# Optimization experiments

Hardware: AMD Instinct MI355X
Metric: run time of the kernel (lower is better)

The kernel has to match this reference:

```python
import jax, jax.numpy as jnp
import numpy as np

B, T, D_IN, D_OUT, H = 128, 128, 64, 64, 1024


def _lstm_cell(x_t, h, c, W_ih, W_hh, b_ih, b_hh):
    # PyTorch LSTMCell: gates = x@W_ih^T + b_ih + h@W_hh^T + b_hh, order [i, f, g, o]
    g = x_t @ W_ih.T + b_ih + h @ W_hh.T + b_hh  # [B, 4H]
    i, f, gg, o = jnp.split(g, 4, axis=-1)
    c_new = jax.nn.sigmoid(f) * c + jax.nn.sigmoid(i) * jnp.tanh(gg)
    h_new = jax.nn.sigmoid(o) * jnp.tanh(c_new)
    return h_new, c_new


def setup_inputs() -> dict:
    key = jax.random.key(0)
    ks = jax.random.split(key, 16)
    s_in = 1.0 / np.sqrt(H)
    inp = {
        "x": jax.random.normal(ks[0], (B, T, D_IN), dtype=jnp.float32),
        "W_ih1": jax.random.normal(ks[1], (4 * H, D_IN), dtype=jnp.float32) * s_in,
        "W_hh1": jax.random.normal(ks[2], (4 * H, H), dtype=jnp.float32) * s_in,
        "b_ih1": jax.random.normal(ks[3], (4 * H,), dtype=jnp.float32) * s_in,
        "b_hh1": jax.random.normal(ks[4], (4 * H,), dtype=jnp.float32) * s_in,
        "W_ih2": jax.random.normal(ks[5], (4 * H, H), dtype=jnp.float32) * s_in,
        "W_hh2": jax.random.normal(ks[6], (4 * H, H), dtype=jnp.float32) * s_in,
        "b_ih2": jax.random.normal(ks[7], (4 * H,), dtype=jnp.float32) * s_in,
        "b_hh2": jax.random.normal(ks[8], (4 * H,), dtype=jnp.float32) * s_in,
        "W_lin": jax.random.normal(ks[9], (D_IN, H), dtype=jnp.float32) * s_in,
        "b_lin": jax.random.normal(ks[10], (D_IN,), dtype=jnp.float32) * s_in,
        "W_hio": jax.random.normal(ks[11], (D_OUT, H), dtype=jnp.float32) * s_in,
        "b_hio": jax.random.normal(ks[12], (D_OUT,), dtype=jnp.float32) * s_in,
        "future": 1,
    }
    return inp


def reference(x, W_ih1, W_hh1, b_ih1, b_hh1, W_ih2, W_hh2, b_ih2, b_hh2,
              W_lin, b_lin, W_hio, b_hio, future):
    b = x.shape[0]
    h1 = jnp.zeros((b, H), x.dtype)
    c1 = jnp.zeros((b, H), x.dtype)
    h2 = jnp.zeros((b, H), x.dtype)
    c2 = jnp.zeros((b, H), x.dtype)

    def step(carry, x_t):
        h1, c1, h2, c2 = carry
        h1, c1 = _lstm_cell(x_t, h1, c1, W_ih1, W_hh1, b_ih1, b_hh1)
        h2, c2 = _lstm_cell(h1, h2, c2, W_ih2, W_hh2, b_ih2, b_hh2)
        return (h1, c1, h2, c2), None

    (h1, c1, h2, c2), _ = jax.lax.scan(step, (h1, c1, h2, c2),
                                       jnp.swapaxes(x, 0, 1))  # scan over T
    output = h2 @ W_lin.T + b_lin  # [B, D_IN] (only last step's value is used)

    for _ in range(int(future)):
        h1, c1 = _lstm_cell(output, h1, c1, W_ih1, W_hh1, b_ih1, b_hh1)
        h2, c2 = _lstm_cell(h1, h2, c2, W_ih2, W_hh2, b_ih2, b_hh2)
        output = h2 @ W_hio.T + b_hio  # [B, D_OUT]

    return output[:, None, :]  # [B, 1, D_OUT]
```

## Files before the change

kernel.cpp:

```cpp
#include <hip/hip_runtime.h>

#define B_   128
#define T_   128
#define DIN  64
#define H_   1024
#define NBLK 256
#define NTHR 512

typedef _Float16 f16;
typedef _Float16 half8 __attribute__((ext_vector_type(8)));
typedef float float4v __attribute__((ext_vector_type(4)));
typedef unsigned uint2v __attribute__((ext_vector_type(2)));
typedef unsigned uint4v __attribute__((ext_vector_type(4)));


#define OFF_W2   34816
#define OFF_SG1  100352
#define OFF_SG2  109056
#define OFF_C1   117760
#define OFF_C2   119808
#define OFF_B1   121856
#define OFF_B2   121920
#define SMEM_BYTES 121984


struct Params {
  const float *x, *Wih1, *Whh1, *bih1, *bhh1, *Wih2, *Whh2, *bih2, *bhh2,
              *Wlin, *blin, *Whio, *bhio;
  const int* fut;
  float* out;
  f16 *x16, *h1a, *h1b, *h2a, *h2b, *ob;
  unsigned *arrive, *rel;
  unsigned *S;
};

__device__ __forceinline__ float sigm(float v) { return 1.f / (1.f + __expf(-v)); }
__device__ __forceinline__ float tanh_(float v) { return 2.f / (1.f + __expf(-2.f * v)) - 1.f; }

__device__ __forceinline__ unsigned get_xcc() {
  unsigned x;
  asm volatile("s_getreg_b32 %0, hwreg(HW_REG_XCC_ID)" : "=s"(x));
  return x & 15u;
}

__device__ __forceinline__ void grid_sync(unsigned* arrive, unsigned* rel, unsigned ph) {
  __syncthreads();
  const int tid = threadIdx.x, bid = blockIdx.x;
  if (bid == 0) {
    if (tid > 0 && tid < NBLK) {
      while (__hip_atomic_load(&arrive[tid], __ATOMIC_RELAXED, __HIP_MEMORY_SCOPE_AGENT) != ph)
        __builtin_amdgcn_s_sleep(8);
    }
    __syncthreads();
    if (tid == 0)
      __hip_atomic_store(rel, ph, __ATOMIC_RELEASE, __HIP_MEMORY_SCOPE_AGENT);
  } else {
    if (tid == 0) {
      __hip_atomic_store(&arrive[bid], ph, __ATOMIC_RELEASE, __HIP_MEMORY_SCOPE_AGENT);
      while (__hip_atomic_load(rel, __ATOMIC_RELAXED, __HIP_MEMORY_SCOPE_AGENT) != ph)
        __builtin_amdgcn_s_sleep(8);
    }
  }
  __syncthreads();
  __builtin_amdgcn_fence(__ATOMIC_ACQUIRE, "agent");
}

__device__ __forceinline__ void fast_sync(unsigned* S, unsigned x, unsigned xtotal,
                                          unsigned nxcd, unsigned ph) {
  __syncthreads();
  if (threadIdx.x == 0) {
    unsigned t = __hip_atomic_fetch_add(&S[x * 32], 1u, __ATOMIC_RELAXED, __HIP_MEMORY_SCOPE_AGENT);
    bool leader = (t % xtotal == 0u);
    if ((t + 1u) % xtotal == 0u) {
      unsigned c = __hip_atomic_fetch_add(&S[512], 1u, __ATOMIC_RELAXED, __HIP_MEMORY_SCOPE_AGENT);
      if ((c + 1u) % nxcd == 0u)
        __hip_atomic_store(&S[544], ph, __ATOMIC_RELAXED, __HIP_MEMORY_SCOPE_AGENT);
      asm volatile("buffer_inv sc0 sc1\n\ts_waitcnt vmcnt(0)" ::: "memory");
      __hip_atomic_store(&S[1088 + x * 32], ph, __ATOMIC_RELAXED, __HIP_MEMORY_SCOPE_AGENT);
    }
    if (leader) {
      while (__hip_atomic_load(&S[544], __ATOMIC_RELAXED, __HIP_MEMORY_SCOPE_AGENT) != ph)
        __builtin_amdgcn_s_sleep(1);
      while (__hip_atomic_load(&S[1088 + x * 32], __ATOMIC_RELAXED, __HIP_MEMORY_SCOPE_AGENT) != ph)
        __builtin_amdgcn_s_sleep(1);
      __hip_atomic_store(&S[576 + x * 32], ph, __ATOMIC_RELAXED, __HIP_MEMORY_SCOPE_AGENT);
      asm volatile("buffer_inv sc0\n\ts_waitcnt vmcnt(0)" ::: "memory");
    } else {
      while (__hip_atomic_load(&S[576 + x * 32], __ATOMIC_RELAXED, __HIP_MEMORY_SCOPE_AGENT) != ph)
        __builtin_amdgcn_s_sleep(2);
      asm volatile("buffer_inv sc0\n\ts_waitcnt vmcnt(0)" ::: "memory");
    }
  }
  __syncthreads();
}

__global__ void __launch_bounds__(NTHR, 1) lstm_k(Params p) {
  extern __shared__ char smem[];
  f16*   W1s  = (f16*)(smem);
  f16*   W2s  = (f16*)(smem + OFF_W2);
  float* Sg1  = (float*)(smem + OFF_SG1);
  float* Sg2  = (float*)(smem + OFF_SG2);
  float* c1   = (float*)(smem + OFF_C1);
  float* c2   = (float*)(smem + OFF_C2);
  float* bs1  = (float*)(smem + OFF_B1);
  float* bs2  = (float*)(smem + OFF_B2);

  const int tid = threadIdx.x, bid = blockIdx.x;
  const int hb  = bid * 4;
  const int fut = p.fut[0];
  const unsigned xcc = get_xcc();
  unsigned* S = p.S;

  if (bid == 0) {
    for (int i = tid; i < 2048; i += NTHR)
      __hip_atomic_store(&S[i], 0u, __ATOMIC_RELAXED, __HIP_MEMORY_SCOPE_AGENT);
  }

  for (int idx = tid; idx < 34 * 512; idx += NTHR) {
    int c = idx >> 9, r = idx & 511;
    int q = r >> 7, colw = (r >> 3) & 15, j = r & 7;
    int k = c * 32 + q * 8 + j;
    int row = (colw >> 2) * H_ + hb + (colw & 3);
    float v = (k < H_) ? p.Whh1[row * H_ + k] : p.Wih1[row * DIN + (k - H_)];
    W1s[idx] = (f16)v;
  }
  for (int idx = tid; idx < 64 * 512; idx += NTHR) {
    int c = idx >> 9, r = idx & 511;
    int q = r >> 7, colw = (r >> 3) & 15, j = r & 7;
    int k = c * 32 + q * 8 + j;
    int row = (colw >> 2) * H_ + hb + (colw & 3);
    float v = (k < H_) ? p.Wih2[row * H_ + k] : p.Whh2[row * H_ + (k - H_)];
    W2s[idx] = (f16)v;
  }
  if (tid < 16) {
    int row = (tid >> 2) * H_ + hb + (tid & 3);
    bs1[tid] = p.bih1[row] + p.bhh1[row];
    bs2[tid] = p.bih2[row] + p.bhh2[row];
  }
  for (int i = tid; i < 512; i += NTHR) { c1[i] = 0.f; c2[i] = 0.f; }
  for (int i = bid * NTHR + tid; i < B_ * T_ * DIN; i += NBLK * NTHR)
    p.x16[i] = (f16)p.x[i];
  for (int i = bid * NTHR + tid; i < B_ * H_; i += NBLK * NTHR) {
    p.h1a[i] = (f16)0.f; p.h1b[i] = (f16)0.f;
    p.h2a[i] = (f16)0.f; p.h2b[i] = (f16)0.f;
  }

  unsigned ph = 1;
  grid_sync(p.arrive, p.rel, ph);
  if (tid == 0)
    __hip_atomic_fetch_add(&S[1600 + xcc], 1u, __ATOMIC_RELAXED, __HIP_MEMORY_SCOPE_AGENT);
  ++ph;
  grid_sync(p.arrive, p.rel, ph);

  unsigned xtotal = __hip_atomic_load(&S[1600 + xcc], __ATOMIC_RELAXED, __HIP_MEMORY_SCOPE_AGENT);
  unsigned nxcd = 0;
  for (int i = 0; i < 16; ++i)
    nxcd += (__hip_atomic_load(&S[1600 + i], __ATOMIC_RELAXED, __HIP_MEMORY_SCOPE_AGENT) != 0u);

  auto gsync = [&]() { ++ph; fast_sync(S, xcc, xtotal, nxcd, ph); };

  const int lane = tid & 63, wv = tid >> 6;
  const int col = lane & 15, quad = lane >> 4;
  const int m0 = wv * 16 + col;
  const int ko = quad * 8;
  const float b1v = bs1[col], b2v = bs2[col];
  const f16* W1f = W1s + lane * 8;
  const f16* W2f = W2s + lane * 8;
  const int hoff = quad * 1024 + m0 * 4;

  f16 *h1c = p.h1a, *h1n = p.h1b, *h2c = p.h2a, *h2n = p.h2b;

  auto lstm_pw = [&](const float* Sgb, float* cst, f16* hn) {
    int mm = tid >> 2, cc = tid & 3;
    float gi = Sgb[mm * 17 + cc],     gf = Sgb[mm * 17 + 4 + cc];
    float gg = Sgb[mm * 17 + 8 + cc], go = Sgb[mm * 17 + 12 + cc];
    float cn = sigm(gf) * cst[tid] + sigm(gi) * tanh_(gg);
    cst[tid] = cn;
    f16 hv = (f16)(sigm(go) * tanh_(cn));
    int v = (int)__builtin_bit_cast(unsigned short, hv);
    int base = lane & ~3;
    int v0 = __shfl(v, base, 64),     v1 = __shfl(v, base + 1, 64);
    int v2 = __shfl(v, base + 2, 64), v3 = __shfl(v, base + 3, 64);
    if (cc == 0) {
      unsigned long long pk = (unsigned long long)(unsigned short)v0
        | ((unsigned long long)(unsigned short)v1 << 16)
        | ((unsigned long long)(unsigned short)v2 << 32)
        | ((unsigned long long)(unsigned short)v3 << 48);
      __hip_atomic_store((unsigned long long*)(hn + bid * 512 + mm * 4), pk,
                         __ATOMIC_RELAXED, __HIP_MEMORY_SCOPE_AGENT);
    }
  };

  auto ldwin = [&](const f16* hX, int j) -> half8 {
    const uint2v* q0 = (const uint2v*)(hX + j * 4096 + hoff);
    const uint2v* q1 = (const uint2v*)(hX + j * 4096 + hoff + 512);
    uint2v u0 = *q0, u1 = *q1;
    uint4v u = {u0[0], u0[1], u1[0], u1[1]};
    return __builtin_bit_cast(half8, u);
  };

  auto phase = [&](bool l1, bool l2, const f16* xp, int xstr) {
    float4v a1 = {b1v, b1v, b1v, b1v};
    float4v a2 = {b2v, b2v, b2v, b2v};

    if (l1) {
      half8 ax0 = *(const half8*)(xp + m0 * xstr + ko);
      half8 ax1 = *(const half8*)(xp + m0 * xstr + 32 + ko);
      a1 = __builtin_amdgcn_mfma_f32_16x16x32_f16(ax0, *(const half8*)(W1f + 32 * 512), a1, 0, 0, 0);
      a1 = __builtin_amdgcn_mfma_f32_16x16x32_f16(ax1, *(const half8*)(W1f + 33 * 512), a1, 0, 0, 0);
    }
    if (l1 && l2) {
      #pragma unroll 4
      for (int j = 0; j < 32; ++j) {
        half8 aw = ldwin(h1c, j);
        a1 = __builtin_amdgcn_mfma_f32_16x16x32_f16(aw, *(const half8*)(W1f + j * 512), a1, 0, 0, 0);
        a2 = __builtin_amdgcn_mfma_f32_16x16x32_f16(aw, *(const half8*)(W2f + j * 512), a2, 0, 0, 0);
      }
    } else if (l1) {
      #pragma unroll 4
      for (int j = 0; j < 32; ++j) {
        half8 aw = ldwin(h1c, j);
        a1 = __builtin_amdgcn_mfma_f32_16x16x32_f16(aw, *(const half8*)(W1f + j * 512), a1, 0, 0, 0);
      }
    } else {
      #pragma unroll 4
      for (int j = 0; j < 32; ++j) {
        half8 aw = ldwin(h1c, j);
        a2 = __builtin_amdgcn_mfma_f32_16x16x32_f16(aw, *(const half8*)(W2f + j * 512), a2, 0, 0, 0);
      }
    }
    if (l2) {
      #pragma unroll 4
      for (int j = 0; j < 32; ++j) {
        half8 aw = ldwin(h2c, j);
        a2 = __builtin_amdgcn_mfma_f32_16x16x32_f16(aw, *(const half8*)(W2f + (32 + j) * 512), a2, 0, 0, 0);
      }
    }

    __syncthreads();
    if (l1) {
      #pragma unroll
      for (int r = 0; r < 4; ++r)
        Sg1[(wv * 16 + quad * 4 + r) * 17 + col] = a1[r];
    }
    if (l2) {
      #pragma unroll
      for (int r = 0; r < 4; ++r)
        Sg2[(wv * 16 + quad * 4 + r) * 17 + col] = a2[r];
    }
    __syncthreads();
    if (l1) lstm_pw(Sg1, c1, h1n);
    if (l2) lstm_pw(Sg2, c2, h2n);
  };

  auto out_phase = [&](const float* W, const float* bv, bool wout) {
    int j = bid & 63, mgp = bid >> 6;
    int rid = tid >> 4, ks = tid & 15;
    int mrow = mgp * 32 + rid;
    const float* wr = W + j * H_ + ks * 64;
    float s = 0.f;
    #pragma unroll
    for (int q = 0; q < 16; ++q) {
      const uint2v* hp = (const uint2v*)(h2c + (ks * 16 + q) * 512 + mrow * 4);
      uint2v u = *hp;
      half8 hv4;
      { uint4v t = {u[0], u[1], 0u, 0u}; hv4 = __builtin_bit_cast(half8, t); }
      s += (float)hv4[0] * wr[q * 4 + 0] + (float)hv4[1] * wr[q * 4 + 1]
         + (float)hv4[2] * wr[q * 4 + 2] + (float)hv4[3] * wr[q * 4 + 3];
    }
    s += __shfl_down(s, 8, 16);
    s += __shfl_down(s, 4, 16);
    s += __shfl_down(s, 2, 16);
    s += __shfl_down(s, 1, 16);
    if (ks == 0) {
      float v = s + bv[j];
      f16 hv = (f16)v;
      __hip_atomic_store((unsigned short*)&p.ob[mrow * 64 + j],
                         __builtin_bit_cast(unsigned short, hv),
                         __ATOMIC_RELAXED, __HIP_MEMORY_SCOPE_AGENT);
      if (wout) p.out[mrow * 64 + j] = v;
    }
  };

  for (int t = -1; t < T_; ++t) {
    bool l1 = (t + 1 < T_), l2 = (t >= 0);
    phase(l1, l2, p.x16 + (t + 1) * DIN, T_ * DIN);
    gsync();
    if (l1) { f16* tm = h1c; h1c = h1n; h1n = tm; }
    if (l2) { f16* tm = h2c; h2c = h2n; h2n = tm; }
  }
  out_phase(p.Wlin, p.blin, fut == 0);
  gsync();
  for (int f = 0; f < fut; ++f) {
    phase(true, false, p.ob, 64);
    gsync();
    { f16* tm = h1c; h1c = h1n; h1n = tm; }
    phase(false, true, p.ob, 64);
    gsync();
    { f16* tm = h2c; h2c = h2n; h2n = tm; }
    out_phase(p.Whio, p.bhio, f == fut - 1);
    gsync();
  }
}

extern "C" void kernel_launch(void* const* d_in, const int* in_sizes, int n_in,
                              void* d_out, int out_size, void* d_ws, size_t ws_size,
                              hipStream_t stream) {
  char* w = (char*)d_ws;
  auto carve = [&](size_t n) { char* r = w; w += (n + 255) & ~(size_t)255; return r; };

  Params p;
  p.x    = (const float*)d_in[0];
  p.Wih1 = (const float*)d_in[1];
  p.Whh1 = (const float*)d_in[2];
  p.bih1 = (const float*)d_in[3];
  p.bhh1 = (const float*)d_in[4];
  p.Wih2 = (const float*)d_in[5];
  p.Whh2 = (const float*)d_in[6];
  p.bih2 = (const float*)d_in[7];
  p.bhh2 = (const float*)d_in[8];
  p.Wlin = (const float*)d_in[9];
  p.blin = (const float*)d_in[10];
  p.Whio = (const float*)d_in[11];
  p.bhio = (const float*)d_in[12];
  p.fut  = (const int*)d_in[13];
  p.out  = (float*)d_out;

  p.x16 = (f16*)carve((size_t)B_ * T_ * DIN * 2);
  p.h1a = (f16*)carve((size_t)B_ * H_ * 2);
  p.h1b = (f16*)carve((size_t)B_ * H_ * 2);
  p.h2a = (f16*)carve((size_t)B_ * H_ * 2);
  p.h2b = (f16*)carve((size_t)B_ * H_ * 2);
  p.ob  = (f16*)carve((size_t)B_ * 64 * 2);
  p.arrive = (unsigned*)carve(NBLK * sizeof(unsigned));
  p.rel    = (unsigned*)carve(256);
  p.S      = (unsigned*)carve(2048 * sizeof(unsigned));

  (void)hipFuncSetAttribute((const void*)lstm_k,
                            hipFuncAttributeMaxDynamicSharedMemorySize, SMEM_BYTES);
  void* args[] = { &p };
  (void)hipLaunchCooperativeKernel((void*)lstm_k, dim3(NBLK), dim3(NTHR),
                                   args, SMEM_BYTES, stream);
}
```

Baseline: 1.902 ms.

## Retile LSTM blocks to 8 hidden units by 64 batch rows, keep Whh2 in registers

Each block now owns 8 hidden columns (32 gate rows) for half the batch instead of 4 columns for the full batch, and the hidden-state layout changes to 8-wide groups so each lane loads one 16-byte half8 instead of two 8-byte pieces. The layer-2 recurrent weights Whh2 move out of LDS into 32 half8 registers per lane, while LDS holds double-width W1 and Wih2 tiles. The intent is fewer and wider global loads of h and a larger weight tile per block. The cost is heavy register pressure (launch bounds changed to 2) and h stores that become per-element 16-bit atomics.

```diff
diff --git a/kernel.cpp b/kernel.cpp
--- a/kernel.cpp
+++ b/kernel.cpp
@@ -10,18 +10,15 @@
 typedef _Float16 f16;
 typedef _Float16 half8 __attribute__((ext_vector_type(8)));
 typedef float float4v __attribute__((ext_vector_type(4)));
-typedef unsigned uint2v __attribute__((ext_vector_type(2)));
-typedef unsigned uint4v __attribute__((ext_vector_type(4)));
-
-
-#define OFF_W2   34816
-#define OFF_SG1  100352
-#define OFF_SG2  109056
-#define OFF_C1   117760
-#define OFF_C2   119808
-#define OFF_B1   121856
-#define OFF_B2   121920
-#define SMEM_BYTES 121984
+
+#define OFF_W2   69632
+#define OFF_SG1  135168
+#define OFF_SG2  143616
+#define OFF_C1   152064
+#define OFF_C2   154112
+#define OFF_B1   156160
+#define OFF_B2   156288
+#define SMEM_BYTES 156416
 
 
 struct Params {
@@ -94,7 +91,7 @@
   __syncthreads();
 }
 
-__global__ void __launch_bounds__(NTHR, 1) lstm_k(Params p) {
+__global__ void __launch_bounds__(NTHR, 2) lstm_k(Params p) {
   extern __shared__ char smem[];
   f16*   W1s  = (f16*)(smem);
   f16*   W2s  = (f16*)(smem + OFF_W2);
@@ -106,34 +103,60 @@
   float* bs2  = (float*)(smem + OFF_B2);
 
   const int tid = threadIdx.x, bid = blockIdx.x;
-  const int hb  = bid * 4;
+  const int cg  = bid >> 1;
+  const int mh  = bid & 1;
   const int fut = p.fut[0];
   const unsigned xcc = get_xcc();
   unsigned* S = p.S;
 
+  const int lane = tid & 63, wv = tid >> 6;
+  const int col = lane & 15, quad = lane >> 4;
+  const int mt = wv & 3;
+  const int nt = wv >> 2;
+  const int mg = mh * 64 + mt * 16 + col;
+  const int hbase = (quad * 2 + mh) * 512 + (mt * 16 + col) * 8;
+
   if (bid == 0) {
     for (int i = tid; i < 2048; i += NTHR)
       __hip_atomic_store(&S[i], 0u, __ATOMIC_RELAXED, __HIP_MEMORY_SCOPE_AGENT);
   }
 
-  for (int idx = tid; idx < 34 * 512; idx += NTHR) {
-    int c = idx >> 9, r = idx & 511;
-    int q = r >> 7, colw = (r >> 3) & 15, j = r & 7;
+  for (int idx = tid; idx < 2 * 34 * 512; idx += NTHR) {
+    int ntl = idx / 17408, rem = idx - ntl * 17408;
+    int c = rem >> 9, r = rem & 511;
+    int q = r >> 7, colL = (r >> 3) & 15, j = r & 7;
     int k = c * 32 + q * 8 + j;
-    int row = (colw >> 2) * H_ + hb + (colw & 3);
+    int gr = ntl * 16 + colL;
+    int row = (gr >> 3) * H_ + cg * 8 + (gr & 7);
     float v = (k < H_) ? p.Whh1[row * H_ + k] : p.Wih1[row * DIN + (k - H_)];
     W1s[idx] = (f16)v;
   }
-  for (int idx = tid; idx < 64 * 512; idx += NTHR) {
-    int c = idx >> 9, r = idx & 511;
-    int q = r >> 7, colw = (r >> 3) & 15, j = r & 7;
+  for (int idx = tid; idx < 2 * 32 * 512; idx += NTHR) {
+    int ntl = idx >> 14, rem = idx & 16383;
+    int c = rem >> 9, r = rem & 511;
+    int q = r >> 7, colL = (r >> 3) & 15, j = r & 7;
     int k = c * 32 + q * 8 + j;
-    int row = (colw >> 2) * H_ + hb + (colw & 3);
-    float v = (k < H_) ? p.Wih2[row * H_ + k] : p.Whh2[row * H_ + (k - H_)];
-    W2s[idx] = (f16)v;
-  }
-  if (tid < 16) {
-    int row = (tid >> 2) * H_ + hb + (tid & 3);
+    int gr = ntl * 16 + colL;
+    int row = (gr >> 3) * H_ + cg * 8 + (gr & 7);
+    W2s[idx] = (f16)p.Wih2[row * H_ + k];
+  }
+  half8 wreg[32];
+  {
+    int gr = nt * 16 + col;
+    int row2 = (gr >> 3) * H_ + cg * 8 + (gr & 7);
+    const float* ws = p.Whh2 + row2 * H_ + quad * 8;
+    #pragma unroll
+    for (int c = 0; c < 32; ++c) {
+      float4v v0 = *(const float4v*)(ws + c * 32);
+      float4v v1 = *(const float4v*)(ws + c * 32 + 4);
+      half8 t;
+      t[0] = (f16)v0[0]; t[1] = (f16)v0[1]; t[2] = (f16)v0[2]; t[3] = (f16)v0[3];
+      t[4] = (f16)v1[0]; t[5] = (f16)v1[1]; t[6] = (f16)v1[2]; t[7] = (f16)v1[3];
+      wreg[c] = t;
+    }
+  }
+  if (tid < 32) {
+    int row = (tid >> 3) * H_ + cg * 8 + (tid & 7);
     bs1[tid] = p.bih1[row] + p.bhh1[row];
     bs2[tid] = p.bih2[row] + p.bhh2[row];
   }
@@ -159,44 +182,26 @@
 
   auto gsync = [&]() { ++ph; fast_sync(S, xcc, xtotal, nxcd, ph); };
 
-  const int lane = tid & 63, wv = tid >> 6;
-  const int col = lane & 15, quad = lane >> 4;
-  const int m0 = wv * 16 + col;
-  const int ko = quad * 8;
-  const float b1v = bs1[col], b2v = bs2[col];
-  const f16* W1f = W1s + lane * 8;
-  const f16* W2f = W2s + lane * 8;
-  const int hoff = quad * 1024 + m0 * 4;
+  const float b1v = bs1[nt * 16 + col], b2v = bs2[nt * 16 + col];
+  const f16* W1f = W1s + nt * (34 * 512) + lane * 8;
+  const f16* W2f = W2s + nt * (32 * 512) + lane * 8;
 
   f16 *h1c = p.h1a, *h1n = p.h1b, *h2c = p.h2a, *h2n = p.h2b;
 
+  auto ldwin = [&](const f16* hX, int j) -> half8 {
+    return *(const half8*)(hX + hbase + j * 4096);
+  };
+
   auto lstm_pw = [&](const float* Sgb, float* cst, f16* hn) {
-    int mm = tid >> 2, cc = tid & 3;
-    float gi = Sgb[mm * 17 + cc],     gf = Sgb[mm * 17 + 4 + cc];
-    float gg = Sgb[mm * 17 + 8 + cc], go = Sgb[mm * 17 + 12 + cc];
+    int r = tid >> 3, c8 = tid & 7;
+    float gi = Sgb[r * 33 + c8],      gf = Sgb[r * 33 + 8 + c8];
+    float gg = Sgb[r * 33 + 16 + c8], go = Sgb[r * 33 + 24 + c8];
     float cn = sigm(gf) * cst[tid] + sigm(gi) * tanh_(gg);
     cst[tid] = cn;
     f16 hv = (f16)(sigm(go) * tanh_(cn));
-    int v = (int)__builtin_bit_cast(unsigned short, hv);
-    int base = lane & ~3;
-    int v0 = __shfl(v, base, 64),     v1 = __shfl(v, base + 1, 64);
-    int v2 = __shfl(v, base + 2, 64), v3 = __shfl(v, base + 3, 64);
-    if (cc == 0) {
-      unsigned long long pk = (unsigned long long)(unsigned short)v0
-        | ((unsigned long long)(unsigned short)v1 << 16)
-        | ((unsigned long long)(unsigned short)v2 << 32)
-        | ((unsigned long long)(unsigned short)v3 << 48);
-      __hip_atomic_store((unsigned long long*)(hn + bid * 512 + mm * 4), pk,
-                         __ATOMIC_RELAXED, __HIP_MEMORY_SCOPE_AGENT);
-    }
-  };
-
-  auto ldwin = [&](const f16* hX, int j) -> half8 {
-    const uint2v* q0 = (const uint2v*)(hX + j * 4096 + hoff);
-    const uint2v* q1 = (const uint2v*)(hX + j * 4096 + hoff + 512);
-    uint2v u0 = *q0, u1 = *q1;
-    uint4v u = {u0[0], u0[1], u1[0], u1[1]};
-    return __builtin_bit_cast(half8, u);
+    __hip_atomic_store((unsigned short*)(hn + bid * 512 + tid),
+                       __builtin_bit_cast(unsigned short, hv),
+                       __ATOMIC_RELAXED, __HIP_MEMORY_SCOPE_AGENT);
   };
 
   auto phase = [&](bool l1, bool l2, const f16* xp, int xstr) {
@@ -204,8 +209,8 @@
     float4v a2 = {b2v, b2v, b2v, b2v};
 
     if (l1) {
-      half8 ax0 = *(const half8*)(xp + m0 * xstr + ko);
-      half8 ax1 = *(const half8*)(xp + m0 * xstr + 32 + ko);
+      half8 ax0 = *(const half8*)(xp + mg * xstr + quad * 8);
+      half8 ax1 = *(const half8*)(xp + mg * xstr + 32 + quad * 8);
       a1 = __builtin_amdgcn_mfma_f32_16x16x32_f16(ax0, *(const half8*)(W1f + 32 * 512), a1, 0, 0, 0);
       a1 = __builtin_amdgcn_mfma_f32_16x16x32_f16(ax1, *(const half8*)(W1f + 33 * 512), a1, 0, 0, 0);
     }
@@ -233,7 +238,7 @@
       #pragma unroll 4
       for (int j = 0; j < 32; ++j) {
         half8 aw = ldwin(h2c, j);
-        a2 = __builtin_amdgcn_mfma_f32_16x16x32_f16(aw, *(const half8*)(W2f + (32 + j) * 512), a2, 0, 0, 0);
+        a2 = __builtin_amdgcn_mfma_f32_16x16x32_f16(aw, wreg[j], a2, 0, 0, 0);
       }
     }
 
@@ -241,12 +246,12 @@
     if (l1) {
       #pragma unroll
       for (int r = 0; r < 4; ++r)
-        Sg1[(wv * 16 + quad * 4 + r) * 17 + col] = a1[r];
+        Sg1[(mt * 16 + quad * 4 + r) * 33 + nt * 16 + col] = a1[r];
     }
     if (l2) {
       #pragma unroll
       for (int r = 0; r < 4; ++r)
-        Sg2[(wv * 16 + quad * 4 + r) * 17 + col] = a2[r];
+        Sg2[(mt * 16 + quad * 4 + r) * 33 + nt * 16 + col] = a2[r];
     }
     __syncthreads();
     if (l1) lstm_pw(Sg1, c1, h1n);
@@ -257,16 +262,15 @@
     int j = bid & 63, mgp = bid >> 6;
     int rid = tid >> 4, ks = tid & 15;
     int mrow = mgp * 32 + rid;
+    int mhp = mrow >> 6, mloc = mrow & 63;
     const float* wr = W + j * H_ + ks * 64;
     float s = 0.f;
     #pragma unroll
-    for (int q = 0; q < 16; ++q) {
-      const uint2v* hp = (const uint2v*)(h2c + (ks * 16 + q) * 512 + mrow * 4);
-      uint2v u = *hp;
-      half8 hv4;
-      { uint4v t = {u[0], u[1], 0u, 0u}; hv4 = __builtin_bit_cast(half8, t); }
-      s += (float)hv4[0] * wr[q * 4 + 0] + (float)hv4[1] * wr[q * 4 + 1]
-         + (float)hv4[2] * wr[q * 4 + 2] + (float)hv4[3] * wr[q * 4 + 3];
+    for (int q = 0; q < 8; ++q) {
+      int cgp = ks * 8 + q;
+      half8 hv = *(const half8*)(h2c + (cgp * 2 + mhp) * 512 + mloc * 8);
+      #pragma unroll
+      for (int i = 0; i < 8; ++i) s += (float)hv[i] * wr[q * 8 + i];
     }
     s += __shfl_down(s, 8, 16);
     s += __shfl_down(s, 4, 16);
```

Result: slower. 2.998 ms (+57.7%).
